# Kernel tuning notes

Hardware: AMD Instinct MI355X
Metric: run time of the kernel (lower is better)

## Reference

```python
import jax, jax.numpy as jnp
import numpy as np

K = 3          # kernel size
PAD = 1        # (K-1)//2, stride=1, dilation=1


def _modulated_deform_conv(depth, offset, mask, w, b):
    """torchvision deform_conv2d with in_ch=out_ch=1, stride=1, pad=1, dil=1.
    depth:  [B,1,H,W]
    offset: [B,2*K*K,H,W]  interleaved (dy, dx) per kernel tap
    mask:   [B,K*K,H,W]    modulation scalars
    w:      [1,1,K,K]      conv weights (ones buffer)
    b:      [1]            bias (zeros buffer)
    """
    B, _, H, W = depth.shape
    kk = K * K
    img = depth[:, 0]                                    # [B,H,W]

    off = offset.reshape(B, kk, 2, H, W)
    dy, dx = off[:, :, 0], off[:, :, 1]                  # [B,kk,H,W]

    # integer tap offsets of the 3x3 kernel
    ky, kx = jnp.meshgrid(jnp.arange(K), jnp.arange(K), indexing='ij')
    ky = ky.reshape(kk).astype(depth.dtype)
    kx = kx.reshape(kk).astype(depth.dtype)

    iy = jnp.arange(H, dtype=depth.dtype)
    ix = jnp.arange(W, dtype=depth.dtype)
    # sampling coords per output pixel per tap: [B,kk,H,W]
    y = iy[None, None, :, None] - PAD + ky[None, :, None, None] + dy
    x = ix[None, None, None, :] - PAD + kx[None, :, None, None] + dx

    y0f = jnp.floor(y); x0f = jnp.floor(x)
    wy = y - y0f; wx = x - x0f                           # frac parts
    y0 = y0f.astype(jnp.int32); x0 = x0f.astype(jnp.int32)
    y1 = y0 + 1;  x1 = x0 + 1

    bidx = jnp.arange(B)[:, None, None, None]

    def corner(yc, xc):
        inb = (yc >= 0) & (yc < H) & (xc >= 0) & (xc < W)
        v = img[bidx, jnp.clip(yc, 0, H - 1), jnp.clip(xc, 0, W - 1)]
        return jnp.where(inb, v, jnp.zeros((), depth.dtype))

    sampled = (corner(y0, x0) * (1 - wy) * (1 - wx)
             + corner(y0, x1) * (1 - wy) * wx
             + corner(y1, x0) * wy * (1 - wx)
             + corner(y1, x1) * wy * wx)                 # [B,kk,H,W]

    wk = w.reshape(1, kk, 1, 1)
    out = jnp.sum(sampled * mask * wk, axis=1) + b[0]    # [B,H,W]
    return out[:, None]                                  # [B,1,H,W]


def setup_inputs() -> dict:
    key = jax.random.key(0)
    k1, k2, k3 = jax.random.split(key, 3)
    B, H, W = 8, 512, 512
    depth  = jax.random.normal(k1, (B, 1, H, W), dtype=jnp.float32)
    weight = jax.random.uniform(k2, (B, K * K, H, W), dtype=jnp.float32)
    offset = jax.random.normal(k3, (B, 2 * K * K, H, W), dtype=jnp.float32)
    w = jnp.ones((1, 1, K, K), dtype=jnp.float32)   # buffer 'w'
    b = jnp.zeros((1,), dtype=jnp.float32)          # buffer 'b'
    return {"depth": depth, "weight": weight, "offset": offset, "w": w, "b": b}


def reference(depth, weight, offset, w, b):
    return _modulated_deform_conv(depth, offset, weight, w, b)
```

## Files before the change

kernel.cpp:

```cpp
#include <hip/hip_runtime.h>


#define KK 9
#define PAD 1

__device__ __forceinline__ float bilin(const float* __restrict__ img,
                                       int H, int W, float y, float x) {
    float y0f = floorf(y);
    float x0f = floorf(x);
    int y0 = (int)y0f;
    int x0 = (int)x0f;
    float wy = y - y0f;
    float wx = x - x0f;
    int y1 = y0 + 1;
    int x1 = x0 + 1;

    bool y0i = (y0 >= 0) & (y0 < H);
    bool y1i = (y1 >= 0) & (y1 < H);
    bool x0i = (x0 >= 0) & (x0 < W);
    bool x1i = (x1 >= 0) & (x1 < W);

    int y0c = min(max(y0, 0), H - 1);
    int y1c = min(max(y1, 0), H - 1);
    int x0c = min(max(x0, 0), W - 1);
    int x1c = min(max(x1, 0), W - 1);

    const float* r0 = img + (long)y0c * W;
    const float* r1 = img + (long)y1c * W;

    float v00 = (y0i & x0i) ? r0[x0c] : 0.0f;
    float v01 = (y0i & x1i) ? r0[x1c] : 0.0f;
    float v10 = (y1i & x0i) ? r1[x0c] : 0.0f;
    float v11 = (y1i & x1i) ? r1[x1c] : 0.0f;

    float omwy = 1.0f - wy;
    float omwx = 1.0f - wx;
    return v00 * omwy * omwx + v01 * omwy * wx + v10 * wy * omwx + v11 * wy * wx;
}

__global__ __launch_bounds__(256) void dcn_kernel(
    const float* __restrict__ depth,
    const float* __restrict__ mask,
    const float* __restrict__ offset,
    const float* __restrict__ w9,
    const float* __restrict__ bias,
    float* __restrict__ out,
    int H, int W) {
    const int HW = H * W;
    const int p = blockIdx.x * blockDim.x + threadIdx.x;
    if (p >= HW) return;
    const int b = blockIdx.y;

    const int y = p / W;
    const int x = p - y * W;

    const float* __restrict__ img = depth + (long)b * HW;
    const float* __restrict__ msk = mask + (long)b * KK * HW + p;
    const float* __restrict__ off = offset + (long)b * 2 * KK * HW + p;

    float acc = bias[0];

    #pragma unroll
    for (int k = 0; k < KK; ++k) {
        const int ky = k / 3;
        const int kx = k - ky * 3;
        const float dy = off[(long)(2 * k) * HW];
        const float dx = off[(long)(2 * k + 1) * HW];
        const float m  = msk[(long)k * HW];
        const float sy = (float)(y - PAD + ky) + dy;
        const float sx = (float)(x - PAD + kx) + dx;
        acc += bilin(img, H, W, sy, sx) * m * w9[k];
    }

    out[(long)b * HW + p] = acc;
}

extern "C" void kernel_launch(void* const* d_in, const int* in_sizes, int n_in,
                              void* d_out, int out_size, void* d_ws, size_t ws_size,
                              hipStream_t stream) {
    const float* depth  = (const float*)d_in[0];
    const float* mask   = (const float*)d_in[1];
    const float* offset = (const float*)d_in[2];
    const float* w9     = (const float*)d_in[3];
    const float* bias   = (const float*)d_in[4];
    float* out = (float*)d_out;

    const int H = 512, W = 512;
    const int HW = H * W;
    const int B = in_sizes[0] / HW;

    dim3 block(256);
    dim3 grid((HW + 255) / 256, B);
    dcn_kernel<<<grid, block, 0, stream>>>(depth, mask, offset, w9, bias, out, H, W);
}
```

Measured before the change: 281.6 us.

## Process four pixels per thread with vectorized nontemporal loads and stores

Each thread now handles four consecutive output pixels and reads offsets and masks as float4 using nontemporal loads, with a float4 nontemporal store for the output. Compile-time H/W constants replace the runtime division and index math, and launch bounds request higher occupancy. The aim is fewer, wider memory transactions on this bandwidth-bound kernel and less streaming data polluting the cache. In exchange there is more register pressure and fewer threads, and the kernel assumes HW is divisible by 1024 with dimensions fixed at 512.

After: 631.0 us. +124.1%, slower.

```diff
diff --git a/kernel.cpp b/kernel.cpp
--- a/kernel.cpp
+++ b/kernel.cpp
@@ -3,9 +3,14 @@
 
 #define KK 9
 #define PAD 1
+#define H 512
+#define W 512
+#define HW (H * W)
+
+typedef float f4 __attribute__((ext_vector_type(4)));
 
 __device__ __forceinline__ float bilin(const float* __restrict__ img,
-                                       int H, int W, float y, float x) {
+                                       float y, float x) {
     float y0f = floorf(y);
     float x0f = floorf(x);
     int y0 = (int)y0f;
@@ -25,54 +30,59 @@
     int x0c = min(max(x0, 0), W - 1);
     int x1c = min(max(x1, 0), W - 1);
 
-    const float* r0 = img + (long)y0c * W;
-    const float* r1 = img + (long)y1c * W;
-
-    float v00 = (y0i & x0i) ? r0[x0c] : 0.0f;
-    float v01 = (y0i & x1i) ? r0[x1c] : 0.0f;
-    float v10 = (y1i & x0i) ? r1[x0c] : 0.0f;
-    float v11 = (y1i & x1i) ? r1[x1c] : 0.0f;
+    float v00 = (y0i & x0i) ? img[y0c * W + x0c] : 0.0f;
+    float v01 = (y0i & x1i) ? img[y0c * W + x1c] : 0.0f;
+    float v10 = (y1i & x0i) ? img[y1c * W + x0c] : 0.0f;
+    float v11 = (y1i & x1i) ? img[y1c * W + x1c] : 0.0f;
 
     float omwy = 1.0f - wy;
     float omwx = 1.0f - wx;
-    return v00 * omwy * omwx + v01 * omwy * wx + v10 * wy * omwx + v11 * wy * wx;
+    return fmaf(v00 * omwy, omwx,
+           fmaf(v01 * omwy, wx,
+           fmaf(v10 * wy,   omwx, v11 * wy * wx)));
 }
 
-__global__ __launch_bounds__(256) void dcn_kernel(
+__global__ __launch_bounds__(256, 4) void dcn_kernel(
     const float* __restrict__ depth,
     const float* __restrict__ mask,
     const float* __restrict__ offset,
     const float* __restrict__ w9,
     const float* __restrict__ bias,
-    float* __restrict__ out,
-    int H, int W) {
-    const int HW = H * W;
-    const int p = blockIdx.x * blockDim.x + threadIdx.x;
-    if (p >= HW) return;
+    float* __restrict__ out) {
+    const int t = blockIdx.x * blockDim.x + threadIdx.x;
+    const int p = t * 4;
     const int b = blockIdx.y;
 
-    const int y = p / W;
-    const int x = p - y * W;
+    const int y  = p >> 9;
+    const int x0 = p & (W - 1);
 
     const float* __restrict__ img = depth + (long)b * HW;
-    const float* __restrict__ msk = mask + (long)b * KK * HW + p;
-    const float* __restrict__ off = offset + (long)b * 2 * KK * HW + p;
+    const f4* __restrict__ msk = (const f4*)(mask   + (long)b * KK * HW + p);
+    const f4* __restrict__ off = (const f4*)(offset + (long)b * 2 * KK * HW + p);
 
-    float acc = bias[0];
+    const float bs = bias[0];
+    float acc0 = bs, acc1 = bs, acc2 = bs, acc3 = bs;
 
     #pragma unroll
     for (int k = 0; k < KK; ++k) {
         const int ky = k / 3;
         const int kx = k - ky * 3;
-        const float dy = off[(long)(2 * k) * HW];
-        const float dx = off[(long)(2 * k + 1) * HW];
-        const float m  = msk[(long)k * HW];
-        const float sy = (float)(y - PAD + ky) + dy;
-        const float sx = (float)(x - PAD + kx) + dx;
-        acc += bilin(img, H, W, sy, sx) * m * w9[k];
+        f4 dy = __builtin_nontemporal_load(&off[(2 * k)     * (HW / 4)]);
+        f4 dx = __builtin_nontemporal_load(&off[(2 * k + 1) * (HW / 4)]);
+        f4 m  = __builtin_nontemporal_load(&msk[k * (HW / 4)]);
+        const float wk = w9[k];
+        const float syb = (float)(y - PAD + ky);
+        const float sxb = (float)(x0 - PAD + kx);
+
+        acc0 = fmaf(bilin(img, syb + dy.x, sxb + 0.0f + dx.x), m.x * wk, acc0);
+        acc1 = fmaf(bilin(img, syb + dy.y, sxb + 1.0f + dx.y), m.y * wk, acc1);
+        acc2 = fmaf(bilin(img, syb + dy.z, sxb + 2.0f + dx.z), m.z * wk, acc2);
+        acc3 = fmaf(bilin(img, syb + dy.w, sxb + 3.0f + dx.w), m.w * wk, acc3);
     }
 
-    out[(long)b * HW + p] = acc;
+    f4 r;
+    r.x = acc0; r.y = acc1; r.z = acc2; r.w = acc3;
+    __builtin_nontemporal_store(r, (f4*)(out + (long)b * HW + p));
 }
 
 extern "C" void kernel_launch(void* const* d_in, const int* in_sizes, int n_in,
@@ -85,11 +95,9 @@
     const float* bias   = (const float*)d_in[4];
     float* out = (float*)d_out;
 
-    const int H = 512, W = 512;
-    const int HW = H * W;
     const int B = in_sizes[0] / HW;
 
     dim3 block(256);
-    dim3 grid((HW + 255) / 256, B);
-    dcn_kernel<<<grid, block, 0, stream>>>(depth, mask, offset, w9, bias, out, H, W);
+    dim3 grid(HW / (256 * 4), B);
+    dcn_kernel<<<grid, block, 0, stream>>>(depth, mask, offset, w9, bias, out);
 }
```
